# Performance work log

Measured on AMD Instinct MI355X. Metric: run time of the kernel, lower is better.

The kernel has to match this reference:

```python
import jax, jax.numpy as jnp
import numpy as np

N, E, SEQ, IN, HID, OUT = 2048, 65536, 5, 32, 64, 16
EPS = 1e-5


def setup_inputs() -> dict:
    ks = jax.random.split(jax.random.key(0), 16)
    def w(k, shape):
        return jax.random.normal(k, shape, jnp.float32) / np.float32(np.sqrt(shape[0]))
    z = lambda n: jnp.zeros((n,), jnp.float32)
    return dict(
        x=jax.random.normal(ks[0], (SEQ, N, IN), jnp.float32),
        edge_weight=jax.random.uniform(ks[1], (E,), jnp.float32),
        Wcz=w(ks[2], (IN, HID)), bcz=z(HID), Wlz=w(ks[3], (2 * HID, HID)), blz=z(HID),
        Wcr=w(ks[4], (IN, HID)), bcr=z(HID), Wlr=w(ks[5], (2 * HID, HID)), blr=z(HID),
        Wch=w(ks[6], (IN, HID)), bch=z(HID), Wlh=w(ks[7], (2 * HID, HID)), blh=z(HID),
        Wred=w(ks[8], (SEQ * HID, HID)), bred=z(HID),
        Wc1=w(ks[9], (HID, HID)), bc1=z(HID), Wc2=w(ks[10], (HID, HID)), bc2=z(HID),
        g1=jnp.ones((HID,), jnp.float32), be1=z(HID),
        g2=jnp.ones((HID,), jnp.float32), be2=z(HID),
        Wout=w(ks[11], (HID, OUT)), bout=z(OUT),
        Wi1=w(ks[12], (2 * HID, HID)), bi1=z(HID),
        Wi2=w(ks[13], (HID, 1)), bi2=z(1),
        edge_index=jax.random.randint(ks[14], (2, E), 0, N),
    )


def _layer_norm(h, g, b):
    mu = jnp.mean(h, -1, keepdims=True)
    var = jnp.mean((h - mu) ** 2, -1, keepdims=True)
    return (h - mu) * jax.lax.rsqrt(var + EPS) * g + b


def _forward(x, edge_weight, Wcz, bcz, Wlz, blz, Wcr, bcr, Wlr, blr,
             Wch, bch, Wlh, blh, Wred, bred, Wc1, bc1, Wc2, bc2,
             g1, be1, g2, be2, Wout, bout, Wi1, bi1, Wi2, bi2, edge_index):
    src, dst = edge_index[0], edge_index[1]
    # GCN symmetric normalization with self-loops (weight 1.0); shared by all convs.
    deg = jax.ops.segment_sum(edge_weight, dst, num_segments=N) + 1.0
    dinv = jax.lax.rsqrt(deg)
    norm = dinv[src] * edge_weight * dinv[dst]  # [E]
    dself = dinv * dinv                          # [N] self-loop coefficient

    def gcn(h, W, b):
        hw = h @ W
        agg = jax.ops.segment_sum(norm[:, None] * hw[src], dst, num_segments=N)
        return agg + dself[:, None] * hw + b

    # TGCN per timestep. The original passes no hidden state, so H resets to 0
    # each call: H_t = (1 - Z) * tanh(candidate); reset gate R is multiplied by
    # H=0 and has no effect (its params get zero gradient, matching torch).
    hs = []
    for t in range(SEQ):  # SEQ=5, fixed small loop
        Zg = jax.nn.sigmoid(gcn(x[t], Wcz, bcz) @ Wlz[:HID] + blz)
        Ht = jnp.tanh(gcn(x[t], Wch, bch) @ Wlh[:HID] + blh)
        hs.append((1.0 - Zg) * Ht)
    h = jnp.stack(hs, axis=1).reshape(N, SEQ * HID)
    h = h @ Wred + bred
    emb = h  # intermediate embeddings for the interaction predictor
    h = gcn(h, Wc1, bc1)
    h = jax.nn.relu(_layer_norm(h, g1, be1))  # dropout = identity in eval
    h = gcn(h, Wc2, bc2)
    h = jax.nn.relu(_layer_norm(h, g2, be2))
    node_pred = h @ Wout + bout
    # InteractionPredictor: cat([e_i, e_j]) @ Wi1 == e_i @ Wi1[:H] + e_j @ Wi1[H:]
    a = emb @ Wi1[:HID]
    bj = emb @ Wi1[HID:]
    hp = jax.nn.relu(a[:, None, :] + bj[None, :, :] + bi1)  # [N, N, HID]
    scores = (hp @ Wi2)[..., 0] + bi2[0]                     # [N, N]
    return node_pred, scores


def reference(x, edge_index, edge_weight, Wcz, bcz, Wlz, blz, Wcr, bcr, Wlr, blr,
              Wch, bch, Wlh, blh, Wred, bred, Wc1, bc1, Wc2, bc2,
              g1, be1, g2, be2, Wout, bout, Wi1, bi1, Wi2, bi2):
    return _forward(x, edge_weight, Wcz, bcz, Wlz, blz, Wcr, bcr, Wlr, blr,
                    Wch, bch, Wlh, blh, Wred, bred, Wc1, bc1, Wc2, bc2,
                    g1, be1, g2, be2, Wout, bout, Wi1, bi1, Wi2, bi2, edge_index)
```

## Files before the change

kernel.cpp:

```cpp
#include <hip/hip_runtime.h>
#include <math.h>

#define N_NODES 2048
#define N_EDGES 65536
#define SEQL 5
#define IN_F 32
#define HID 64
#define OUT_F 16
#define LN_EPS 1e-5f
#define CAP 128

__global__ __launch_bounds__(256) void k_build(
        const int* __restrict__ ei, const float* __restrict__ ew,
        const float* __restrict__ Wcz, const float* __restrict__ Wlz,
        const float* __restrict__ bcz, const float* __restrict__ blz,
        const float* __restrict__ Wch, const float* __restrict__ Wlh,
        const float* __restrict__ bch, const float* __restrict__ blh,
        float* __restrict__ deg, int* __restrict__ cnt, float2* __restrict__ cedge,
        float* __restrict__ Wzp, float* __restrict__ Whp, float* __restrict__ bUV){
    int b = blockIdx.x, t = threadIdx.x;
    if (b < 256){
        int e = b * 256 + t;
        int s = ei[e], d = ei[N_EDGES + e];
        float wv = ew[e];
        atomicAdd(&deg[d], wv);
        int pos = atomicAdd(&cnt[d], 1);
        if (pos < CAP){
            float2 v;
            v.x = __int_as_float(s);
            v.y = wv;
            cedge[(d << 7) + pos] = v;
        }
    } else {
        const float* Wc = (b == 256) ? Wcz : Wch;
        const float* Wl = (b == 256) ? Wlz : Wlh;
        const float* bc = (b == 256) ? bcz : bch;
        const float* bl = (b == 256) ? blz : blh;
        float* Wp = (b == 256) ? Wzp : Whp;
        for (int idx = t; idx < IN_F*HID; idx += 256){
            int i = idx >> 6, f = idx & 63;
            float s = 0.f;
            #pragma unroll 8
            for (int k = 0; k < HID; ++k) s += Wc[i*HID+k] * Wl[k*HID+f];
            Wp[idx] = s;
        }
        if (t < HID){
            float s = bl[t];
            for (int k = 0; k < HID; ++k) s += bc[k] * Wl[k*HID+t];
            bUV[(b-256)*HID + t] = s;
        }
    }
}

__global__ __launch_bounds__(320) void k_gate(const float* __restrict__ x,
        const float* __restrict__ deg, const int* __restrict__ cnt,
        const float2* __restrict__ cedge,
        const float* __restrict__ bUV, const float* __restrict__ Wzp, const float* __restrict__ Whp,
        const float* __restrict__ Wred, const float* __restrict__ bred,
        const float* __restrict__ Wi1, const float* __restrict__ bi1, const float* __restrict__ Wc1,
        float* __restrict__ ag, float* __restrict__ bjp, float* __restrict__ hw1y){
    int n = blockIdx.x;
    int tid = threadIdx.x;
    __shared__ float part[40*SEQL*IN_F];
    __shared__ float axs[SEQL][IN_F];
    __shared__ float hs[SEQL][HID];
    __shared__ float pw[SEQL][HID];
    __shared__ float hemb[HID];
    const int slot = tid >> 3, fl = tid & 7;
    const int f = tid & 63, t = tid >> 6;
    int m = min(cnt[n], CAP);
    float dvn = 1.f / sqrtf(deg[n] + 1.f);
    float dsn = dvn * dvn;
    const float4* X4 = (const float4*)x;
    float4 a0 = {0,0,0,0}, a1 = {0,0,0,0}, a2 = {0,0,0,0}, a3 = {0,0,0,0}, a4 = {0,0,0,0};
    for (int p = slot; p < m; p += 40){
        float2 ed = cedge[(n << 7) + p];
        int s = __float_as_int(ed.x);
        float c = ed.y * (1.f / sqrtf(deg[s] + 1.f));
        float4 x0 = X4[(0*N_NODES + s)*8 + fl];
        float4 x1 = X4[(1*N_NODES + s)*8 + fl];
        float4 x2 = X4[(2*N_NODES + s)*8 + fl];
        float4 x3 = X4[(3*N_NODES + s)*8 + fl];
        float4 x4v= X4[(4*N_NODES + s)*8 + fl];
        a0.x += c*x0.x; a0.y += c*x0.y; a0.z += c*x0.z; a0.w += c*x0.w;
        a1.x += c*x1.x; a1.y += c*x1.y; a1.z += c*x1.z; a1.w += c*x1.w;
        a2.x += c*x2.x; a2.y += c*x2.y; a2.z += c*x2.z; a2.w += c*x2.w;
        a3.x += c*x3.x; a3.y += c*x3.y; a3.z += c*x3.z; a3.w += c*x3.w;
        a4.x += c*x4v.x; a4.y += c*x4v.y; a4.z += c*x4v.z; a4.w += c*x4v.w;
    }
    *(float4*)&part[(slot*SEQL + 0)*IN_F + fl*4] = a0;
    *(float4*)&part[(slot*SEQL + 1)*IN_F + fl*4] = a1;
    *(float4*)&part[(slot*SEQL + 2)*IN_F + fl*4] = a2;
    *(float4*)&part[(slot*SEQL + 3)*IN_F + fl*4] = a3;
    *(float4*)&part[(slot*SEQL + 4)*IN_F + fl*4] = a4;
    __syncthreads();
    if (tid < SEQL*IN_F){
        int tt = tid >> 5, ff = tid & 31;
        float ps = 0.f;
        #pragma unroll 8
        for (int sl = 0; sl < 40; ++sl) ps += part[(sl*SEQL + tt)*IN_F + ff];
        axs[tt][ff] = dsn * x[(tt*N_NODES + n)*IN_F + ff] + dvn * ps;
    }
    __syncthreads();
    {
        float zz = bUV[f], hh = bUV[HID + f];
        #pragma unroll
        for (int i = 0; i < IN_F; ++i){
            float a = axs[t][i];
            zz += a * Wzp[i*HID + f];
            hh += a * Whp[i*HID + f];
        }
        float z = 1.f / (1.f + expf(-zz));
        hs[t][f] = (1.f - z) * tanhf(hh);
    }
    __syncthreads();
    {   float pp = 0.f;
        #pragma unroll
        for (int k = 0; k < HID; ++k) pp += hs[t][k] * Wred[(t*HID + k)*HID + f];
        pw[t][f] = pp;
    }
    __syncthreads();
    if (tid < HID){
        float hr = bred[tid];
        #pragma unroll
        for (int t2 = 0; t2 < SEQL; ++t2) hr += pw[t2][tid];
        hemb[tid] = hr;
    }
    __syncthreads();
    if (t < 3){
        const float* W = (t == 0) ? Wi1 : (t == 1) ? (Wi1 + HID*HID) : Wc1;
        float acc = (t == 1) ? bi1[f] : 0.f;
        #pragma unroll
        for (int k = 0; k < HID; ++k) acc += hemb[k] * W[k*HID + f];
        if (t == 2) acc *= dvn;
        float* O = (t == 0) ? ag : (t == 1) ? bjp : hw1y;
        O[n*HID + f] = acc;
    }
}

__global__ __launch_bounds__(512) void k_gcn1s(
        const float* __restrict__ hw1y, const float* __restrict__ deg,
        const int* __restrict__ cnt, const float2* __restrict__ cedge,
        const float* __restrict__ bc1, const float* __restrict__ g1, const float* __restrict__ be1,
        const float* __restrict__ Wc2, float* __restrict__ hw2y,
        const float* __restrict__ ag, const float* __restrict__ bjp,
        const float* __restrict__ Wi2, const float* __restrict__ bi2,
        float* __restrict__ outs){
    int blk = blockIdx.x;
    int tid = threadIdx.x;
    if (blk < 256){
        int w = tid >> 6, l = tid & 63;
        int n = (blk << 3) + w;
        int slot = l >> 4, fl = l & 15;
        int m = min(cnt[n], CAP);
        float dv = 1.f / sqrtf(deg[n] + 1.f);
        const float4* H4 = (const float4*)hw1y;
        float4 acc = {0.f,0.f,0.f,0.f};
        if (slot == 0) acc = H4[n*16 + fl];
        for (int p = slot; p < m; p += 4){
            float2 ed = cedge[(n << 7) + p];
            int s = __float_as_int(ed.x); float c = ed.y;
            float4 h = H4[s*16 + fl];
            acc.x += c*h.x; acc.y += c*h.y; acc.z += c*h.z; acc.w += c*h.w;
        }
        acc.x += __shfl_xor(acc.x, 16); acc.y += __shfl_xor(acc.y, 16);
        acc.z += __shfl_xor(acc.z, 16); acc.w += __shfl_xor(acc.w, 16);
        acc.x += __shfl_xor(acc.x, 32); acc.y += __shfl_xor(acc.y, 32);
        acc.z += __shfl_xor(acc.z, 32); acc.w += __shfl_xor(acc.w, 32);
        float4 b4 = ((const float4*)bc1)[fl];
        float4 g;
        g.x = b4.x + dv*acc.x; g.y = b4.y + dv*acc.y;
        g.z = b4.z + dv*acc.z; g.w = b4.w + dv*acc.w;
        float s4 = g.x + g.y + g.z + g.w;
        s4 += __shfl_xor(s4, 1); s4 += __shfl_xor(s4, 2);
        s4 += __shfl_xor(s4, 4); s4 += __shfl_xor(s4, 8);
        float mu = s4 * (1.f/64.f);
        float4 d;
        d.x = g.x - mu; d.y = g.y - mu; d.z = g.z - mu; d.w = g.w - mu;
        float v4 = d.x*d.x + d.y*d.y + d.z*d.z + d.w*d.w;
        v4 += __shfl_xor(v4, 1); v4 += __shfl_xor(v4, 2);
        v4 += __shfl_xor(v4, 4); v4 += __shfl_xor(v4, 8);
        float rs = 1.f / sqrtf(v4 * (1.f/64.f) + LN_EPS);
        float4 gm = ((const float4*)g1)[fl], be = ((const float4*)be1)[fl];
        float4 h4;
        h4.x = fmaxf(d.x*rs*gm.x + be.x, 0.f);
        h4.y = fmaxf(d.y*rs*gm.y + be.y, 0.f);
        h4.z = fmaxf(d.z*rs*gm.z + be.z, 0.f);
        h4.w = fmaxf(d.w*rs*gm.w + be.w, 0.f);
        float o = 0.f;
        #pragma unroll 4
        for (int gk = 0; gk < 16; ++gk){
            float hb0 = __shfl(h4.x, gk);
            float hb1 = __shfl(h4.y, gk);
            float hb2 = __shfl(h4.z, gk);
            float hb3 = __shfl(h4.w, gk);
            o += hb0 * Wc2[(4*gk+0)*HID + l];
            o += hb1 * Wc2[(4*gk+1)*HID + l];
            o += hb2 * Wc2[(4*gk+2)*HID + l];
            o += hb3 * Wc2[(4*gk+3)*HID + l];
        }
        hw2y[n*HID + l] = dv * o;
    } else {
        __shared__ float bs[64*65];
        __shared__ float wv[64];
        int tl = blk - 256;
        int j0 = (tl & 31) * 64;
        int i0 = (tl >> 5) * 32;
        for (int idx = tid; idx < 4096; idx += 512){
            int jj = idx >> 6, f = idx & 63;
            bs[jj*65 + f] = bjp[(j0 + jj)*HID + f];
        }
        if (tid < 64) wv[tid] = Wi2[tid];
        __syncthreads();
        int tj = tid & 63;
        int w = __builtin_amdgcn_readfirstlane(tid >> 6);
        const float* ar = ag + (i0 + w*4)*HID;
        float bi2v = bi2[0];
        float acc0 = 0.f, acc1 = 0.f, acc2 = 0.f, acc3 = 0.f;
        #pragma unroll
        for (int f = 0; f < 64; ++f){
            float bv = bs[tj*65 + f];
            float wf = wv[f];
            acc0 += fmaxf(ar[       f] + bv, 0.f) * wf;
            acc1 += fmaxf(ar[ 64 +  f] + bv, 0.f) * wf;
            acc2 += fmaxf(ar[128 +  f] + bv, 0.f) * wf;
            acc3 += fmaxf(ar[192 +  f] + bv, 0.f) * wf;
        }
        long ro = (long)(i0 + w*4) * N_NODES + j0 + tj;
        outs[ro                ] = acc0 + bi2v;
        outs[ro +     N_NODES  ] = acc1 + bi2v;
        outs[ro + 2L* N_NODES  ] = acc2 + bi2v;
        outs[ro + 3L* N_NODES  ] = acc3 + bi2v;
    }
}

__global__ __launch_bounds__(512) void k_gcn2s(
        const float* __restrict__ hw2y, const float* __restrict__ deg,
        const int* __restrict__ cnt, const float2* __restrict__ cedge,
        const float* __restrict__ bc2, const float* __restrict__ g2, const float* __restrict__ be2,
        const float* __restrict__ Wout, const float* __restrict__ bout,
        const float* __restrict__ ag, const float* __restrict__ bjp,
        const float* __restrict__ Wi2, const float* __restrict__ bi2,
        float* __restrict__ outp, float* __restrict__ outs){
    int blk = blockIdx.x;
    int tid = threadIdx.x;
    if (blk < 256){
        int w = tid >> 6, l = tid & 63;
        int n = (blk << 3) + w;
        int slot = l >> 4, fl = l & 15;
        int m = min(cnt[n], CAP);
        float dv = 1.f / sqrtf(deg[n] + 1.f);
        const float4* H4 = (const float4*)hw2y;
        float4 acc = {0.f,0.f,0.f,0.f};
        if (slot == 0) acc = H4[n*16 + fl];
        for (int p = slot; p < m; p += 4){
            float2 ed = cedge[(n << 7) + p];
            int s = __float_as_int(ed.x); float c = ed.y;
            float4 h = H4[s*16 + fl];
            acc.x += c*h.x; acc.y += c*h.y; acc.z += c*h.z; acc.w += c*h.w;
        }
        acc.x += __shfl_xor(acc.x, 16); acc.y += __shfl_xor(acc.y, 16);
        acc.z += __shfl_xor(acc.z, 16); acc.w += __shfl_xor(acc.w, 16);
        acc.x += __shfl_xor(acc.x, 32); acc.y += __shfl_xor(acc.y, 32);
        acc.z += __shfl_xor(acc.z, 32); acc.w += __shfl_xor(acc.w, 32);
        float4 b4 = ((const float4*)bc2)[fl];
        float4 g;
        g.x = b4.x + dv*acc.x; g.y = b4.y + dv*acc.y;
        g.z = b4.z + dv*acc.z; g.w = b4.w + dv*acc.w;
        float s4 = g.x + g.y + g.z + g.w;
        s4 += __shfl_xor(s4, 1); s4 += __shfl_xor(s4, 2);
        s4 += __shfl_xor(s4, 4); s4 += __shfl_xor(s4, 8);
        float mu = s4 * (1.f/64.f);
        float4 d;
        d.x = g.x - mu; d.y = g.y - mu; d.z = g.z - mu; d.w = g.w - mu;
        float v4 = d.x*d.x + d.y*d.y + d.z*d.z + d.w*d.w;
        v4 += __shfl_xor(v4, 1); v4 += __shfl_xor(v4, 2);
        v4 += __shfl_xor(v4, 4); v4 += __shfl_xor(v4, 8);
        float rs = 1.f / sqrtf(v4 * (1.f/64.f) + LN_EPS);
        float4 gm = ((const float4*)g2)[fl], be = ((const float4*)be2)[fl];
        float4 h4;
        h4.x = fmaxf(d.x*rs*gm.x + be.x, 0.f);
        h4.y = fmaxf(d.y*rs*gm.y + be.y, 0.f);
        h4.z = fmaxf(d.z*rs*gm.z + be.z, 0.f);
        h4.w = fmaxf(d.w*rs*gm.w + be.w, 0.f);
        int f2 = l & 15;
        float o = bout[f2];
        #pragma unroll 4
        for (int gk = 0; gk < 16; ++gk){
            float hb0 = __shfl(h4.x, gk);
            float hb1 = __shfl(h4.y, gk);
            float hb2 = __shfl(h4.z, gk);
            float hb3 = __shfl(h4.w, gk);
            o += hb0 * Wout[(4*gk+0)*OUT_F + f2];
            o += hb1 * Wout[(4*gk+1)*OUT_F + f2];
            o += hb2 * Wout[(4*gk+2)*OUT_F + f2];
            o += hb3 * Wout[(4*gk+3)*OUT_F + f2];
        }
        if (slot == 0) outp[n*OUT_F + f2] = o;
    } else {
        __shared__ float bs[64*65];
        __shared__ float wv[64];
        int tl = blk - 256 + 1024;
        int j0 = (tl & 31) * 64;
        int i0 = (tl >> 5) * 32;
        for (int idx = tid; idx < 4096; idx += 512){
            int jj = idx >> 6, f = idx & 63;
            bs[jj*65 + f] = bjp[(j0 + jj)*HID + f];
        }
        if (tid < 64) wv[tid] = Wi2[tid];
        __syncthreads();
        int tj = tid & 63;
        int w = __builtin_amdgcn_readfirstlane(tid >> 6);
        const float* ar = ag + (i0 + w*4)*HID;
        float bi2v = bi2[0];
        float acc0 = 0.f, acc1 = 0.f, acc2 = 0.f, acc3 = 0.f;
        #pragma unroll
        for (int f = 0; f < 64; ++f){
            float bv = bs[tj*65 + f];
            float wf = wv[f];
            acc0 += fmaxf(ar[       f] + bv, 0.f) * wf;
            acc1 += fmaxf(ar[ 64 +  f] + bv, 0.f) * wf;
            acc2 += fmaxf(ar[128 +  f] + bv, 0.f) * wf;
            acc3 += fmaxf(ar[192 +  f] + bv, 0.f) * wf;
        }
        long ro = (long)(i0 + w*4) * N_NODES + j0 + tj;
        outs[ro                ] = acc0 + bi2v;
        outs[ro +     N_NODES  ] = acc1 + bi2v;
        outs[ro + 2L* N_NODES  ] = acc2 + bi2v;
        outs[ro + 3L* N_NODES  ] = acc3 + bi2v;
    }
}

extern "C" void kernel_launch(void* const* d_in, const int* in_sizes, int n_in,
                              void* d_out, int out_size, void* d_ws, size_t ws_size,
                              hipStream_t stream){
    const float* x   = (const float*)d_in[0];
    const float* ew  = (const float*)d_in[1];
    const float* Wcz = (const float*)d_in[2];  const float* bcz = (const float*)d_in[3];
    const float* Wlz = (const float*)d_in[4];  const float* blz = (const float*)d_in[5];
    const float* Wch = (const float*)d_in[10]; const float* bch = (const float*)d_in[11];
    const float* Wlh = (const float*)d_in[12]; const float* blh = (const float*)d_in[13];
    const float* Wred= (const float*)d_in[14]; const float* bred= (const float*)d_in[15];
    const float* Wc1 = (const float*)d_in[16]; const float* bc1 = (const float*)d_in[17];
    const float* Wc2 = (const float*)d_in[18]; const float* bc2 = (const float*)d_in[19];
    const float* g1  = (const float*)d_in[20]; const float* be1 = (const float*)d_in[21];
    const float* g2  = (const float*)d_in[22]; const float* be2 = (const float*)d_in[23];
    const float* Wout= (const float*)d_in[24]; const float* bout= (const float*)d_in[25];
    const float* Wi1 = (const float*)d_in[26]; const float* bi1 = (const float*)d_in[27];
    const float* Wi2 = (const float*)d_in[28]; const float* bi2 = (const float*)d_in[29];
    const int*  ei  = (const int*)d_in[30];

    float* w = (float*)d_ws;
    float* deg   = w;
    int*   cnt   = (int*)(w + 2048);
    float2* cedge= (float2*)(w + 4096);
    float* Wzp   = w + 528384;
    float* Whp   = w + 530432;
    float* bUV   = w + 532480;
    float* ag    = w + 532608;
    float* bjp   = w + 663680;
    float* hw1y  = w + 794752;
    float* hw2y  = w + 925824;

    hipMemsetAsync(deg, 0, 16384, stream);
    k_build<<<258, 256, 0, stream>>>(ei, ew, Wcz, Wlz, bcz, blz, Wch, Wlh, bch, blh,
                                     deg, cnt, cedge, Wzp, Whp, bUV);
    k_gate<<<N_NODES, 320, 0, stream>>>(x, deg, cnt, cedge, bUV, Wzp, Whp,
                                        Wred, bred, Wi1, bi1, Wc1, ag, bjp, hw1y);
    k_gcn1s<<<256 + 1024, 512, 0, stream>>>(hw1y, deg, cnt, cedge, bc1, g1, be1,
                                            Wc2, hw2y, ag, bjp, Wi2, bi2,
                                            (float*)d_out + N_NODES*OUT_F);
    k_gcn2s<<<256 + 1024, 512, 0, stream>>>(hw2y, deg, cnt, cedge, bc2, g2, be2,
                                            Wout, bout, ag, bjp, Wi2, bi2,
                                            (float*)d_out, (float*)d_out + N_NODES*OUT_F);
}
```

Measured before the change: 198.4 us.

## Fuse four kernels into one persistent kernel with software grid barriers

Result: slower. 388.3 us (+95.7%).

```diff
diff --git a/kernel.cpp b/kernel.cpp
--- a/kernel.cpp
+++ b/kernel.cpp
@@ -9,18 +9,213 @@
 #define OUT_F 16
 #define LN_EPS 1e-5f
 #define CAP 128
-
-__global__ __launch_bounds__(256) void k_build(
-        const int* __restrict__ ei, const float* __restrict__ ew,
-        const float* __restrict__ Wcz, const float* __restrict__ Wlz,
-        const float* __restrict__ bcz, const float* __restrict__ blz,
-        const float* __restrict__ Wch, const float* __restrict__ Wlh,
-        const float* __restrict__ bch, const float* __restrict__ blh,
-        float* __restrict__ deg, int* __restrict__ cnt, float2* __restrict__ cedge,
-        float* __restrict__ Wzp, float* __restrict__ Whp, float* __restrict__ bUV){
-    int b = blockIdx.x, t = threadIdx.x;
-    if (b < 256){
-        int e = b * 256 + t;
+#define NBLK 512
+
+__device__ __forceinline__ void gbar(unsigned* bar, unsigned target){
+    __syncthreads();
+    if (threadIdx.x == 0){
+        __threadfence();
+        atomicAdd(bar, 1u);
+        while (atomicAdd(bar, 0u) < target) __builtin_amdgcn_s_sleep(2);
+        __threadfence();
+    }
+    __syncthreads();
+}
+
+union SMem {
+    struct {
+        float part[2][16][SEQL][IN_F];
+        float axs[2][SEQL][IN_F];
+        float hs[2][SEQL][HID];
+        float pw[2][SEQL][HID];
+        float hemb[2][HID];
+    } g;
+    struct { float bs[64*65]; float wv[64]; } s;
+};
+
+__device__ __forceinline__ void score_tile(int tl, int tid, SMem& sm,
+        const float* __restrict__ ag, const float* __restrict__ bjp,
+        const float* __restrict__ Wi2, const float* __restrict__ bi2,
+        float* __restrict__ outs){
+    int j0 = (tl & 31) * 64;
+    int i0 = (tl >> 5) * 32;
+    __syncthreads();
+    for (int idx = tid; idx < 4096; idx += 256){
+        int jj = idx >> 6, f = idx & 63;
+        sm.s.bs[jj*65 + f] = bjp[(j0 + jj)*HID + f];
+    }
+    if (tid < 64) sm.s.wv[tid] = Wi2[tid];
+    __syncthreads();
+    int tj = tid & 63;
+    int w = __builtin_amdgcn_readfirstlane(tid >> 6);
+    const float* ar = ag + (i0 + w*8)*HID;
+    float bi2v = bi2[0];
+    float a0=0.f,a1=0.f,a2=0.f,a3=0.f,a4=0.f,a5=0.f,a6=0.f,a7=0.f;
+    #pragma unroll 16
+    for (int f = 0; f < 64; ++f){
+        float bv = sm.s.bs[tj*65 + f];
+        float wf = sm.s.wv[f];
+        a0 += fmaxf(ar[0*HID + f] + bv, 0.f) * wf;
+        a1 += fmaxf(ar[1*HID + f] + bv, 0.f) * wf;
+        a2 += fmaxf(ar[2*HID + f] + bv, 0.f) * wf;
+        a3 += fmaxf(ar[3*HID + f] + bv, 0.f) * wf;
+        a4 += fmaxf(ar[4*HID + f] + bv, 0.f) * wf;
+        a5 += fmaxf(ar[5*HID + f] + bv, 0.f) * wf;
+        a6 += fmaxf(ar[6*HID + f] + bv, 0.f) * wf;
+        a7 += fmaxf(ar[7*HID + f] + bv, 0.f) * wf;
+    }
+    long ro = (long)(i0 + w*8) * N_NODES + j0 + tj;
+    outs[ro              ] = a0 + bi2v;
+    outs[ro + 1L*N_NODES ] = a1 + bi2v;
+    outs[ro + 2L*N_NODES ] = a2 + bi2v;
+    outs[ro + 3L*N_NODES ] = a3 + bi2v;
+    outs[ro + 4L*N_NODES ] = a4 + bi2v;
+    outs[ro + 5L*N_NODES ] = a5 + bi2v;
+    outs[ro + 6L*N_NODES ] = a6 + bi2v;
+    outs[ro + 7L*N_NODES ] = a7 + bi2v;
+}
+
+__device__ __forceinline__ void gcn1_node(int n, int l,
+        const float* __restrict__ deg, const int* __restrict__ cnt,
+        const float2* __restrict__ cedge, const float* __restrict__ hw1y,
+        const float* __restrict__ bc1, const float* __restrict__ g1,
+        const float* __restrict__ be1, const float* __restrict__ Wc2,
+        float* __restrict__ hw2y){
+    int slot = l >> 4, fl = l & 15;
+    int m = min(cnt[n], CAP);
+    float dv = 1.f / sqrtf(deg[n] + 1.f);
+    const float4* H4 = (const float4*)hw1y;
+    float4 acc = {0.f,0.f,0.f,0.f};
+    if (slot == 0) acc = H4[n*16 + fl];
+    for (int p = slot; p < m; p += 4){
+        float2 ed = cedge[(n << 7) + p];
+        int s = __float_as_int(ed.x); float c = ed.y;
+        float4 h = H4[s*16 + fl];
+        acc.x += c*h.x; acc.y += c*h.y; acc.z += c*h.z; acc.w += c*h.w;
+    }
+    acc.x += __shfl_xor(acc.x, 16); acc.y += __shfl_xor(acc.y, 16);
+    acc.z += __shfl_xor(acc.z, 16); acc.w += __shfl_xor(acc.w, 16);
+    acc.x += __shfl_xor(acc.x, 32); acc.y += __shfl_xor(acc.y, 32);
+    acc.z += __shfl_xor(acc.z, 32); acc.w += __shfl_xor(acc.w, 32);
+    float4 b4 = ((const float4*)bc1)[fl];
+    float4 g;
+    g.x = b4.x + dv*acc.x; g.y = b4.y + dv*acc.y;
+    g.z = b4.z + dv*acc.z; g.w = b4.w + dv*acc.w;
+    float s4 = g.x + g.y + g.z + g.w;
+    s4 += __shfl_xor(s4, 1); s4 += __shfl_xor(s4, 2);
+    s4 += __shfl_xor(s4, 4); s4 += __shfl_xor(s4, 8);
+    float mu = s4 * (1.f/64.f);
+    float4 d;
+    d.x = g.x - mu; d.y = g.y - mu; d.z = g.z - mu; d.w = g.w - mu;
+    float v4 = d.x*d.x + d.y*d.y + d.z*d.z + d.w*d.w;
+    v4 += __shfl_xor(v4, 1); v4 += __shfl_xor(v4, 2);
+    v4 += __shfl_xor(v4, 4); v4 += __shfl_xor(v4, 8);
+    float rs = 1.f / sqrtf(v4 * (1.f/64.f) + LN_EPS);
+    float4 gm = ((const float4*)g1)[fl], be = ((const float4*)be1)[fl];
+    float4 h4;
+    h4.x = fmaxf(d.x*rs*gm.x + be.x, 0.f);
+    h4.y = fmaxf(d.y*rs*gm.y + be.y, 0.f);
+    h4.z = fmaxf(d.z*rs*gm.z + be.z, 0.f);
+    h4.w = fmaxf(d.w*rs*gm.w + be.w, 0.f);
+    float o = 0.f;
+    #pragma unroll 4
+    for (int gk = 0; gk < 16; ++gk){
+        float hb0 = __shfl(h4.x, gk);
+        float hb1 = __shfl(h4.y, gk);
+        float hb2 = __shfl(h4.z, gk);
+        float hb3 = __shfl(h4.w, gk);
+        o += hb0 * Wc2[(4*gk+0)*HID + l];
+        o += hb1 * Wc2[(4*gk+1)*HID + l];
+        o += hb2 * Wc2[(4*gk+2)*HID + l];
+        o += hb3 * Wc2[(4*gk+3)*HID + l];
+    }
+    hw2y[n*HID + l] = dv * o;
+}
+
+__device__ __forceinline__ void gcn2_node(int n, int l,
+        const float* __restrict__ deg, const int* __restrict__ cnt,
+        const float2* __restrict__ cedge, const float* __restrict__ hw2y,
+        const float* __restrict__ bc2, const float* __restrict__ g2,
+        const float* __restrict__ be2, const float* __restrict__ Wout,
+        const float* __restrict__ bout, float* __restrict__ outp){
+    int slot = l >> 4, fl = l & 15;
+    int m = min(cnt[n], CAP);
+    float dv = 1.f / sqrtf(deg[n] + 1.f);
+    const float4* H4 = (const float4*)hw2y;
+    float4 acc = {0.f,0.f,0.f,0.f};
+    if (slot == 0) acc = H4[n*16 + fl];
+    for (int p = slot; p < m; p += 4){
+        float2 ed = cedge[(n << 7) + p];
+        int s = __float_as_int(ed.x); float c = ed.y;
+        float4 h = H4[s*16 + fl];
+        acc.x += c*h.x; acc.y += c*h.y; acc.z += c*h.z; acc.w += c*h.w;
+    }
+    acc.x += __shfl_xor(acc.x, 16); acc.y += __shfl_xor(acc.y, 16);
+    acc.z += __shfl_xor(acc.z, 16); acc.w += __shfl_xor(acc.w, 16);
+    acc.x += __shfl_xor(acc.x, 32); acc.y += __shfl_xor(acc.y, 32);
+    acc.z += __shfl_xor(acc.z, 32); acc.w += __shfl_xor(acc.w, 32);
+    float4 b4 = ((const float4*)bc2)[fl];
+    float4 g;
+    g.x = b4.x + dv*acc.x; g.y = b4.y + dv*acc.y;
+    g.z = b4.z + dv*acc.z; g.w = b4.w + dv*acc.w;
+    float s4 = g.x + g.y + g.z + g.w;
+    s4 += __shfl_xor(s4, 1); s4 += __shfl_xor(s4, 2);
+    s4 += __shfl_xor(s4, 4); s4 += __shfl_xor(s4, 8);
+    float mu = s4 * (1.f/64.f);
+    float4 d;
+    d.x = g.x - mu; d.y = g.y - mu; d.z = g.z - mu; d.w = g.w - mu;
+    float v4 = d.x*d.x + d.y*d.y + d.z*d.z + d.w*d.w;
+    v4 += __shfl_xor(v4, 1); v4 += __shfl_xor(v4, 2);
+    v4 += __shfl_xor(v4, 4); v4 += __shfl_xor(v4, 8);
+    float rs = 1.f / sqrtf(v4 * (1.f/64.f) + LN_EPS);
+    float4 gm = ((const float4*)g2)[fl], be = ((const float4*)be2)[fl];
+    float4 h4;
+    h4.x = fmaxf(d.x*rs*gm.x + be.x, 0.f);
+    h4.y = fmaxf(d.y*rs*gm.y + be.y, 0.f);
+    h4.z = fmaxf(d.z*rs*gm.z + be.z, 0.f);
+    h4.w = fmaxf(d.w*rs*gm.w + be.w, 0.f);
+    int f2 = l & 15;
+    float o = bout[f2];
+    #pragma unroll 4
+    for (int gk = 0; gk < 16; ++gk){
+        float hb0 = __shfl(h4.x, gk);
+        float hb1 = __shfl(h4.y, gk);
+        float hb2 = __shfl(h4.z, gk);
+        float hb3 = __shfl(h4.w, gk);
+        o += hb0 * Wout[(4*gk+0)*OUT_F + f2];
+        o += hb1 * Wout[(4*gk+1)*OUT_F + f2];
+        o += hb2 * Wout[(4*gk+2)*OUT_F + f2];
+        o += hb3 * Wout[(4*gk+3)*OUT_F + f2];
+    }
+    if (slot == 0) outp[n*OUT_F + f2] = o;
+}
+
+__global__ __launch_bounds__(256, 2) void k_mega(
+        const float* __restrict__ x, const float* __restrict__ ew, const int* __restrict__ ei,
+        const float* __restrict__ Wcz, const float* __restrict__ bcz,
+        const float* __restrict__ Wlz, const float* __restrict__ blz,
+        const float* __restrict__ Wch, const float* __restrict__ bch,
+        const float* __restrict__ Wlh, const float* __restrict__ blh,
+        const float* __restrict__ Wred, const float* __restrict__ bred,
+        const float* __restrict__ Wc1, const float* __restrict__ bc1,
+        const float* __restrict__ Wc2, const float* __restrict__ bc2,
+        const float* __restrict__ g1, const float* __restrict__ be1,
+        const float* __restrict__ g2, const float* __restrict__ be2,
+        const float* __restrict__ Wout, const float* __restrict__ bout,
+        const float* __restrict__ Wi1, const float* __restrict__ bi1,
+        const float* __restrict__ Wi2, const float* __restrict__ bi2,
+        float* __restrict__ deg, int* __restrict__ cnt, unsigned* __restrict__ bar,
+        float2* __restrict__ cedge,
+        float* __restrict__ Wzp, float* __restrict__ Whp, float* __restrict__ bUV,
+        float* __restrict__ ag, float* __restrict__ bjp,
+        float* __restrict__ hw1y, float* __restrict__ hw2y,
+        float* __restrict__ outp, float* __restrict__ outs){
+    __shared__ SMem sm;
+    const int blk = blockIdx.x, tid = threadIdx.x;
+    const int w = tid >> 6, l = tid & 63;
+
+    if (blk < 256){
+        int e = blk * 256 + tid;
         int s = ei[e], d = ei[N_EDGES + e];
         float wv = ew[e];
         atomicAdd(&deg[d], wv);
@@ -31,304 +226,145 @@
             v.y = wv;
             cedge[(d << 7) + pos] = v;
         }
-    } else {
-        const float* Wc = (b == 256) ? Wcz : Wch;
-        const float* Wl = (b == 256) ? Wlz : Wlh;
-        const float* bc = (b == 256) ? bcz : bch;
-        const float* bl = (b == 256) ? blz : blh;
-        float* Wp = (b == 256) ? Wzp : Whp;
-        for (int idx = t; idx < IN_F*HID; idx += 256){
+    } else if (blk < 258){
+        const float* Wc = (blk == 256) ? Wcz : Wch;
+        const float* Wl = (blk == 256) ? Wlz : Wlh;
+        float* Wp = (blk == 256) ? Wzp : Whp;
+        for (int idx = tid; idx < IN_F*HID; idx += 256){
             int i = idx >> 6, f = idx & 63;
             float s = 0.f;
             #pragma unroll 8
             for (int k = 0; k < HID; ++k) s += Wc[i*HID+k] * Wl[k*HID+f];
             Wp[idx] = s;
         }
-        if (t < HID){
-            float s = bl[t];
-            for (int k = 0; k < HID; ++k) s += bc[k] * Wl[k*HID+t];
-            bUV[(b-256)*HID + t] = s;
-        }
-    }
-}
-
-__global__ __launch_bounds__(320) void k_gate(const float* __restrict__ x,
-        const float* __restrict__ deg, const int* __restrict__ cnt,
-        const float2* __restrict__ cedge,
-        const float* __restrict__ bUV, const float* __restrict__ Wzp, const float* __restrict__ Whp,
-        const float* __restrict__ Wred, const float* __restrict__ bred,
-        const float* __restrict__ Wi1, const float* __restrict__ bi1, const float* __restrict__ Wc1,
-        float* __restrict__ ag, float* __restrict__ bjp, float* __restrict__ hw1y){
-    int n = blockIdx.x;
-    int tid = threadIdx.x;
-    __shared__ float part[40*SEQL*IN_F];
-    __shared__ float axs[SEQL][IN_F];
-    __shared__ float hs[SEQL][HID];
-    __shared__ float pw[SEQL][HID];
-    __shared__ float hemb[HID];
-    const int slot = tid >> 3, fl = tid & 7;
-    const int f = tid & 63, t = tid >> 6;
-    int m = min(cnt[n], CAP);
-    float dvn = 1.f / sqrtf(deg[n] + 1.f);
-    float dsn = dvn * dvn;
-    const float4* X4 = (const float4*)x;
-    float4 a0 = {0,0,0,0}, a1 = {0,0,0,0}, a2 = {0,0,0,0}, a3 = {0,0,0,0}, a4 = {0,0,0,0};
-    for (int p = slot; p < m; p += 40){
-        float2 ed = cedge[(n << 7) + p];
-        int s = __float_as_int(ed.x);
-        float c = ed.y * (1.f / sqrtf(deg[s] + 1.f));
-        float4 x0 = X4[(0*N_NODES + s)*8 + fl];
-        float4 x1 = X4[(1*N_NODES + s)*8 + fl];
-        float4 x2 = X4[(2*N_NODES + s)*8 + fl];
-        float4 x3 = X4[(3*N_NODES + s)*8 + fl];
-        float4 x4v= X4[(4*N_NODES + s)*8 + fl];
-        a0.x += c*x0.x; a0.y += c*x0.y; a0.z += c*x0.z; a0.w += c*x0.w;
-        a1.x += c*x1.x; a1.y += c*x1.y; a1.z += c*x1.z; a1.w += c*x1.w;
-        a2.x += c*x2.x; a2.y += c*x2.y; a2.z += c*x2.z; a2.w += c*x2.w;
-        a3.x += c*x3.x; a3.y += c*x3.y; a3.z += c*x3.z; a3.w += c*x3.w;
-        a4.x += c*x4v.x; a4.y += c*x4v.y; a4.z += c*x4v.z; a4.w += c*x4v.w;
-    }
-    *(float4*)&part[(slot*SEQL + 0)*IN_F + fl*4] = a0;
-    *(float4*)&part[(slot*SEQL + 1)*IN_F + fl*4] = a1;
-    *(float4*)&part[(slot*SEQL + 2)*IN_F + fl*4] = a2;
-    *(float4*)&part[(slot*SEQL + 3)*IN_F + fl*4] = a3;
-    *(float4*)&part[(slot*SEQL + 4)*IN_F + fl*4] = a4;
-    __syncthreads();
-    if (tid < SEQL*IN_F){
-        int tt = tid >> 5, ff = tid & 31;
-        float ps = 0.f;
-        #pragma unroll 8
-        for (int sl = 0; sl < 40; ++sl) ps += part[(sl*SEQL + tt)*IN_F + ff];
-        axs[tt][ff] = dsn * x[(tt*N_NODES + n)*IN_F + ff] + dvn * ps;
-    }
-    __syncthreads();
-    {
-        float zz = bUV[f], hh = bUV[HID + f];
-        #pragma unroll
-        for (int i = 0; i < IN_F; ++i){
-            float a = axs[t][i];
-            zz += a * Wzp[i*HID + f];
-            hh += a * Whp[i*HID + f];
-        }
-        float z = 1.f / (1.f + expf(-zz));
-        hs[t][f] = (1.f - z) * tanhf(hh);
-    }
-    __syncthreads();
-    {   float pp = 0.f;
-        #pragma unroll
-        for (int k = 0; k < HID; ++k) pp += hs[t][k] * Wred[(t*HID + k)*HID + f];
-        pw[t][f] = pp;
-    }
-    __syncthreads();
-    if (tid < HID){
-        float hr = bred[tid];
-        #pragma unroll
-        for (int t2 = 0; t2 < SEQL; ++t2) hr += pw[t2][tid];
-        hemb[tid] = hr;
-    }
-    __syncthreads();
-    if (t < 3){
-        const float* W = (t == 0) ? Wi1 : (t == 1) ? (Wi1 + HID*HID) : Wc1;
-        float acc = (t == 1) ? bi1[f] : 0.f;
-        #pragma unroll
-        for (int k = 0; k < HID; ++k) acc += hemb[k] * W[k*HID + f];
-        if (t == 2) acc *= dvn;
-        float* O = (t == 0) ? ag : (t == 1) ? bjp : hw1y;
-        O[n*HID + f] = acc;
-    }
-}
-
-__global__ __launch_bounds__(512) void k_gcn1s(
-        const float* __restrict__ hw1y, const float* __restrict__ deg,
-        const int* __restrict__ cnt, const float2* __restrict__ cedge,
-        const float* __restrict__ bc1, const float* __restrict__ g1, const float* __restrict__ be1,
-        const float* __restrict__ Wc2, float* __restrict__ hw2y,
-        const float* __restrict__ ag, const float* __restrict__ bjp,
-        const float* __restrict__ Wi2, const float* __restrict__ bi2,
-        float* __restrict__ outs){
-    int blk = blockIdx.x;
-    int tid = threadIdx.x;
+    } else if (blk == 258){
+        if (tid < 128){
+            int which = tid >> 6, f = tid & 63;
+            const float* Wl = which ? Wlh : Wlz;
+            const float* bc = which ? bch : bcz;
+            const float* bl = which ? blh : blz;
+            float s = bl[f];
+            for (int k = 0; k < HID; ++k) s += bc[k] * Wl[k*HID+f];
+            bUV[which*HID + f] = s;
+        }
+    }
+    gbar(bar, NBLK);
+
+    for (int pass = 0; pass < 2; ++pass){
+        int nb = (blk << 2) + pass*2;
+        {
+            int half = tid >> 7;
+            int r = tid & 127;
+            int slot = r >> 3, fl = r & 7;
+            int n = nb + half;
+            int m = min(cnt[n], CAP);
+            const float4* X4 = (const float4*)x;
+            float4 a0={0,0,0,0},a1={0,0,0,0},a2={0,0,0,0},a3={0,0,0,0},a4={0,0,0,0};
+            for (int p = slot; p < m; p += 16){
+                float2 edv = cedge[(n << 7) + p];
+                int s = __float_as_int(edv.x);
+                float c = edv.y * (1.f / sqrtf(deg[s] + 1.f));
+                float4 x0 = X4[(0*N_NODES + s)*8 + fl];
+                float4 x1 = X4[(1*N_NODES + s)*8 + fl];
+                float4 x2 = X4[(2*N_NODES + s)*8 + fl];
+                float4 x3 = X4[(3*N_NODES + s)*8 + fl];
+                float4 x4v= X4[(4*N_NODES + s)*8 + fl];
+                a0.x += c*x0.x; a0.y += c*x0.y; a0.z += c*x0.z; a0.w += c*x0.w;
+                a1.x += c*x1.x; a1.y += c*x1.y; a1.z += c*x1.z; a1.w += c*x1.w;
+                a2.x += c*x2.x; a2.y += c*x2.y; a2.z += c*x2.z; a2.w += c*x2.w;
+                a3.x += c*x3.x; a3.y += c*x3.y; a3.z += c*x3.z; a3.w += c*x3.w;
+                a4.x += c*x4v.x; a4.y += c*x4v.y; a4.z += c*x4v.z; a4.w += c*x4v.w;
+            }
+            *(float4*)&sm.g.part[half][slot][0][fl*4] = a0;
+            *(float4*)&sm.g.part[half][slot][1][fl*4] = a1;
+            *(float4*)&sm.g.part[half][slot][2][fl*4] = a2;
+            *(float4*)&sm.g.part[half][slot][3][fl*4] = a3;
+            *(float4*)&sm.g.part[half][slot][4][fl*4] = a4;
+        }
+        __syncthreads();
+        for (int idx = tid; idx < 2*SEQL*IN_F; idx += 256){
+            int nn = idx >= 160 ? 1 : 0;
+            int rem = idx - nn*160;
+            int tt = rem >> 5, ff = rem & 31;
+            int n = nb + nn;
+            float dv = 1.f / sqrtf(deg[n] + 1.f);
+            float ps = 0.f;
+            #pragma unroll
+            for (int sl = 0; sl < 16; ++sl) ps += sm.g.part[nn][sl][tt][ff];
+            sm.g.axs[nn][tt][ff] = dv*dv * x[(tt*N_NODES + n)*IN_F + ff] + dv * ps;
+        }
+        __syncthreads();
+        for (int task = w; task < 10; task += 4){
+            int nn = task >= 5 ? 1 : 0;
+            int t = task - nn*5;
+            float zz = bUV[l], hh = bUV[HID + l];
+            #pragma unroll 8
+            for (int i = 0; i < IN_F; ++i){
+                float a = sm.g.axs[nn][t][i];
+                zz += a * Wzp[i*HID + l];
+                hh += a * Whp[i*HID + l];
+            }
+            float z = 1.f / (1.f + expf(-zz));
+            sm.g.hs[nn][t][l] = (1.f - z) * tanhf(hh);
+        }
+        __syncthreads();
+        for (int task = w; task < 10; task += 4){
+            int nn = task >= 5 ? 1 : 0;
+            int t = task - nn*5;
+            float pp = 0.f;
+            #pragma unroll 8
+            for (int k = 0; k < HID; ++k) pp += sm.g.hs[nn][t][k] * Wred[(t*HID + k)*HID + l];
+            sm.g.pw[nn][t][l] = pp;
+        }
+        __syncthreads();
+        if (tid < 2*HID){
+            int nn = tid >> 6, ff = tid & 63;
+            float hr = bred[ff];
+            #pragma unroll
+            for (int t2 = 0; t2 < SEQL; ++t2) hr += sm.g.pw[nn][t2][ff];
+            sm.g.hemb[nn][ff] = hr;
+        }
+        __syncthreads();
+        for (int task = w; task < 6; task += 4){
+            int nn = task >= 3 ? 1 : 0;
+            int o = task - nn*3;
+            int n = nb + nn;
+            const float* W = (o == 0) ? Wi1 : (o == 1) ? (Wi1 + HID*HID) : Wc1;
+            float acc = (o == 1) ? bi1[l] : 0.f;
+            #pragma unroll 8
+            for (int k = 0; k < HID; ++k) acc += sm.g.hemb[nn][k] * W[k*HID + l];
+            if (o == 2) acc *= 1.f / sqrtf(deg[n] + 1.f);
+            float* O = (o == 0) ? ag : (o == 1) ? bjp : hw1y;
+            O[n*HID + l] = acc;
+        }
+        __syncthreads();
+    }
+    gbar(bar, 2*NBLK);
+
     if (blk < 256){
-        int w = tid >> 6, l = tid & 63;
-        int n = (blk << 3) + w;
-        int slot = l >> 4, fl = l & 15;
-        int m = min(cnt[n], CAP);
-        float dv = 1.f / sqrtf(deg[n] + 1.f);
-        const float4* H4 = (const float4*)hw1y;
-        float4 acc = {0.f,0.f,0.f,0.f};
-        if (slot == 0) acc = H4[n*16 + fl];
-        for (int p = slot; p < m; p += 4){
-            float2 ed = cedge[(n << 7) + p];
-            int s = __float_as_int(ed.x); float c = ed.y;
-            float4 h = H4[s*16 + fl];
-            acc.x += c*h.x; acc.y += c*h.y; acc.z += c*h.z; acc.w += c*h.w;
-        }
-        acc.x += __shfl_xor(acc.x, 16); acc.y += __shfl_xor(acc.y, 16);
-        acc.z += __shfl_xor(acc.z, 16); acc.w += __shfl_xor(acc.w, 16);
-        acc.x += __shfl_xor(acc.x, 32); acc.y += __shfl_xor(acc.y, 32);
-        acc.z += __shfl_xor(acc.z, 32); acc.w += __shfl_xor(acc.w, 32);
-        float4 b4 = ((const float4*)bc1)[fl];
-        float4 g;
-        g.x = b4.x + dv*acc.x; g.y = b4.y + dv*acc.y;
-        g.z = b4.z + dv*acc.z; g.w = b4.w + dv*acc.w;
-        float s4 = g.x + g.y + g.z + g.w;
-        s4 += __shfl_xor(s4, 1); s4 += __shfl_xor(s4, 2);
-        s4 += __shfl_xor(s4, 4); s4 += __shfl_xor(s4, 8);
-        float mu = s4 * (1.f/64.f);
-        float4 d;
-        d.x = g.x - mu; d.y = g.y - mu; d.z = g.z - mu; d.w = g.w - mu;
-        float v4 = d.x*d.x + d.y*d.y + d.z*d.z + d.w*d.w;
-        v4 += __shfl_xor(v4, 1); v4 += __shfl_xor(v4, 2);
-        v4 += __shfl_xor(v4, 4); v4 += __shfl_xor(v4, 8);
-        float rs = 1.f / sqrtf(v4 * (1.f/64.f) + LN_EPS);
-        float4 gm = ((const float4*)g1)[fl], be = ((const float4*)be1)[fl];
-        float4 h4;
-        h4.x = fmaxf(d.x*rs*gm.x + be.x, 0.f);
-        h4.y = fmaxf(d.y*rs*gm.y + be.y, 0.f);
-        h4.z = fmaxf(d.z*rs*gm.z + be.z, 0.f);
-        h4.w = fmaxf(d.w*rs*gm.w + be.w, 0.f);
-        float o = 0.f;
-        #pragma unroll 4
-        for (int gk = 0; gk < 16; ++gk){
-            float hb0 = __shfl(h4.x, gk);
-            float hb1 = __shfl(h4.y, gk);
-            float hb2 = __shfl(h4.z, gk);
-            float hb3 = __shfl(h4.w, gk);
-            o += hb0 * Wc2[(4*gk+0)*HID + l];
-            o += hb1 * Wc2[(4*gk+1)*HID + l];
-            o += hb2 * Wc2[(4*gk+2)*HID + l];
-            o += hb3 * Wc2[(4*gk+3)*HID + l];
-        }
-        hw2y[n*HID + l] = dv * o;
+        for (int rep = 0; rep < 2; ++rep){
+            int n = (blk << 3) + rep*4 + w;
+            gcn1_node(n, l, deg, cnt, cedge, hw1y, bc1, g1, be1, Wc2, hw2y);
+        }
     } else {
-        __shared__ float bs[64*65];
-        __shared__ float wv[64];
-        int tl = blk - 256;
-        int j0 = (tl & 31) * 64;
-        int i0 = (tl >> 5) * 32;
-        for (int idx = tid; idx < 4096; idx += 512){
-            int jj = idx >> 6, f = idx & 63;
-            bs[jj*65 + f] = bjp[(j0 + jj)*HID + f];
-        }
-        if (tid < 64) wv[tid] = Wi2[tid];
-        __syncthreads();
-        int tj = tid & 63;
-        int w = __builtin_amdgcn_readfirstlane(tid >> 6);
-        const float* ar = ag + (i0 + w*4)*HID;
-        float bi2v = bi2[0];
-        float acc0 = 0.f, acc1 = 0.f, acc2 = 0.f, acc3 = 0.f;
-        #pragma unroll
-        for (int f = 0; f < 64; ++f){
-            float bv = bs[tj*65 + f];
-            float wf = wv[f];
-            acc0 += fmaxf(ar[       f] + bv, 0.f) * wf;
-            acc1 += fmaxf(ar[ 64 +  f] + bv, 0.f) * wf;
-            acc2 += fmaxf(ar[128 +  f] + bv, 0.f) * wf;
-            acc3 += fmaxf(ar[192 +  f] + bv, 0.f) * wf;
-        }
-        long ro = (long)(i0 + w*4) * N_NODES + j0 + tj;
-        outs[ro                ] = acc0 + bi2v;
-        outs[ro +     N_NODES  ] = acc1 + bi2v;
-        outs[ro + 2L* N_NODES  ] = acc2 + bi2v;
-        outs[ro + 3L* N_NODES  ] = acc3 + bi2v;
-    }
-}
-
-__global__ __launch_bounds__(512) void k_gcn2s(
-        const float* __restrict__ hw2y, const float* __restrict__ deg,
-        const int* __restrict__ cnt, const float2* __restrict__ cedge,
-        const float* __restrict__ bc2, const float* __restrict__ g2, const float* __restrict__ be2,
-        const float* __restrict__ Wout, const float* __restrict__ bout,
-        const float* __restrict__ ag, const float* __restrict__ bjp,
-        const float* __restrict__ Wi2, const float* __restrict__ bi2,
-        float* __restrict__ outp, float* __restrict__ outs){
-    int blk = blockIdx.x;
-    int tid = threadIdx.x;
+        score_tile((blk - 256)*2,     tid, sm, ag, bjp, Wi2, bi2, outs);
+        score_tile((blk - 256)*2 + 1, tid, sm, ag, bjp, Wi2, bi2, outs);
+    }
+    gbar(bar, 3*NBLK);
+
     if (blk < 256){
-        int w = tid >> 6, l = tid & 63;
-        int n = (blk << 3) + w;
-        int slot = l >> 4, fl = l & 15;
-        int m = min(cnt[n], CAP);
-        float dv = 1.f / sqrtf(deg[n] + 1.f);
-        const float4* H4 = (const float4*)hw2y;
-        float4 acc = {0.f,0.f,0.f,0.f};
-        if (slot == 0) acc = H4[n*16 + fl];
-        for (int p = slot; p < m; p += 4){
-            float2 ed = cedge[(n << 7) + p];
-            int s = __float_as_int(ed.x); float c = ed.y;
-            float4 h = H4[s*16 + fl];
-            acc.x += c*h.x; acc.y += c*h.y; acc.z += c*h.z; acc.w += c*h.w;
-        }
-        acc.x += __shfl_xor(acc.x, 16); acc.y += __shfl_xor(acc.y, 16);
-        acc.z += __shfl_xor(acc.z, 16); acc.w += __shfl_xor(acc.w, 16);
-        acc.x += __shfl_xor(acc.x, 32); acc.y += __shfl_xor(acc.y, 32);
-        acc.z += __shfl_xor(acc.z, 32); acc.w += __shfl_xor(acc.w, 32);
-        float4 b4 = ((const float4*)bc2)[fl];
-        float4 g;
-        g.x = b4.x + dv*acc.x; g.y = b4.y + dv*acc.y;
-        g.z = b4.z + dv*acc.z; g.w = b4.w + dv*acc.w;
-        float s4 = g.x + g.y + g.z + g.w;
-        s4 += __shfl_xor(s4, 1); s4 += __shfl_xor(s4, 2);
-        s4 += __shfl_xor(s4, 4); s4 += __shfl_xor(s4, 8);
-        float mu = s4 * (1.f/64.f);
-        float4 d;
-        d.x = g.x - mu; d.y = g.y - mu; d.z = g.z - mu; d.w = g.w - mu;
-        float v4 = d.x*d.x + d.y*d.y + d.z*d.z + d.w*d.w;
-        v4 += __shfl_xor(v4, 1); v4 += __shfl_xor(v4, 2);
-        v4 += __shfl_xor(v4, 4); v4 += __shfl_xor(v4, 8);
-        float rs = 1.f / sqrtf(v4 * (1.f/64.f) + LN_EPS);
-        float4 gm = ((const float4*)g2)[fl], be = ((const float4*)be2)[fl];
-        float4 h4;
-        h4.x = fmaxf(d.x*rs*gm.x + be.x, 0.f);
-        h4.y = fmaxf(d.y*rs*gm.y + be.y, 0.f);
-        h4.z = fmaxf(d.z*rs*gm.z + be.z, 0.f);
-        h4.w = fmaxf(d.w*rs*gm.w + be.w, 0.f);
-        int f2 = l & 15;
-        float o = bout[f2];
-        #pragma unroll 4
-        for (int gk = 0; gk < 16; ++gk){
-            float hb0 = __shfl(h4.x, gk);
-            float hb1 = __shfl(h4.y, gk);
-            float hb2 = __shfl(h4.z, gk);
-            float hb3 = __shfl(h4.w, gk);
-            o += hb0 * Wout[(4*gk+0)*OUT_F + f2];
-            o += hb1 * Wout[(4*gk+1)*OUT_F + f2];
-            o += hb2 * Wout[(4*gk+2)*OUT_F + f2];
-            o += hb3 * Wout[(4*gk+3)*OUT_F + f2];
-        }
-        if (slot == 0) outp[n*OUT_F + f2] = o;
+        for (int rep = 0; rep < 2; ++rep){
+            int n = (blk << 3) + rep*4 + w;
+            gcn2_node(n, l, deg, cnt, cedge, hw2y, bc2, g2, be2, Wout, bout, outp);
+        }
     } else {
-        __shared__ float bs[64*65];
-        __shared__ float wv[64];
-        int tl = blk - 256 + 1024;
-        int j0 = (tl & 31) * 64;
-        int i0 = (tl >> 5) * 32;
-        for (int idx = tid; idx < 4096; idx += 512){
-            int jj = idx >> 6, f = idx & 63;
-            bs[jj*65 + f] = bjp[(j0 + jj)*HID + f];
-        }
-        if (tid < 64) wv[tid] = Wi2[tid];
-        __syncthreads();
-        int tj = tid & 63;
-        int w = __builtin_amdgcn_readfirstlane(tid >> 6);
-        const float* ar = ag + (i0 + w*4)*HID;
-        float bi2v = bi2[0];
-        float acc0 = 0.f, acc1 = 0.f, acc2 = 0.f, acc3 = 0.f;
-        #pragma unroll
-        for (int f = 0; f < 64; ++f){
-            float bv = bs[tj*65 + f];
-            float wf = wv[f];
-            acc0 += fmaxf(ar[       f] + bv, 0.f) * wf;
-            acc1 += fmaxf(ar[ 64 +  f] + bv, 0.f) * wf;
-            acc2 += fmaxf(ar[128 +  f] + bv, 0.f) * wf;
-            acc3 += fmaxf(ar[192 +  f] + bv, 0.f) * wf;
-        }
-        long ro = (long)(i0 + w*4) * N_NODES + j0 + tj;
-        outs[ro                ] = acc0 + bi2v;
-        outs[ro +     N_NODES  ] = acc1 + bi2v;
-        outs[ro + 2L* N_NODES  ] = acc2 + bi2v;
-        outs[ro + 3L* N_NODES  ] = acc3 + bi2v;
-    }
+        score_tile(512 + (blk - 256), tid, sm, ag, bjp, Wi2, bi2, outs);
+    }
+
+    score_tile(768 + blk,        tid, sm, ag, bjp, Wi2, bi2, outs);
+    score_tile(768 + NBLK + blk, tid, sm, ag, bjp, Wi2, bi2, outs);
+    if (blk < 256)
+        score_tile(768 + 2*NBLK + blk, tid, sm, ag, bjp, Wi2, bi2, outs);
 }
 
 extern "C" void kernel_launch(void* const* d_in, const int* in_sizes, int n_in,
@@ -353,24 +389,21 @@
     float* w = (float*)d_ws;
     float* deg   = w;
     int*   cnt   = (int*)(w + 2048);
-    float2* cedge= (float2*)(w + 4096);
-    float* Wzp   = w + 528384;
-    float* Whp   = w + 530432;
-    float* bUV   = w + 532480;
-    float* ag    = w + 532608;
-    float* bjp   = w + 663680;
-    float* hw1y  = w + 794752;
-    float* hw2y  = w + 925824;
-
-    hipMemsetAsync(deg, 0, 16384, stream);
-    k_build<<<258, 256, 0, stream>>>(ei, ew, Wcz, Wlz, bcz, blz, Wch, Wlh, bch, blh,
-                                     deg, cnt, cedge, Wzp, Whp, bUV);
-    k_gate<<<N_NODES, 320, 0, stream>>>(x, deg, cnt, cedge, bUV, Wzp, Whp,
-                                        Wred, bred, Wi1, bi1, Wc1, ag, bjp, hw1y);
-    k_gcn1s<<<256 + 1024, 512, 0, stream>>>(hw1y, deg, cnt, cedge, bc1, g1, be1,
-                                            Wc2, hw2y, ag, bjp, Wi2, bi2,
-                                            (float*)d_out + N_NODES*OUT_F);
-    k_gcn2s<<<256 + 1024, 512, 0, stream>>>(hw2y, deg, cnt, cedge, bc2, g2, be2,
-                                            Wout, bout, ag, bjp, Wi2, bi2,
-                                            (float*)d_out, (float*)d_out + N_NODES*OUT_F);
-}
+    unsigned* bar= (unsigned*)(w + 4096);
+    float2* cedge= (float2*)(w + 4112);
+    float* Wzp   = w + 528400;
+    float* Whp   = w + 530448;
+    float* bUV   = w + 532496;
+    float* ag    = w + 532624;
+    float* bjp   = w + 663696;
+    float* hw1y  = w + 794768;
+    float* hw2y  = w + 925840;
+    float* outp  = (float*)d_out;
+    float* outs  = (float*)d_out + N_NODES*OUT_F;
+
+    hipMemsetAsync(deg, 0, 16448, stream);
+    k_mega<<<NBLK, 256, 0, stream>>>(x, ew, ei,
+        Wcz, bcz, Wlz, blz, Wch, bch, Wlh, blh, Wred, bred,
+        Wc1, bc1, Wc2, bc2, g1, be1, g2, be2, Wout, bout, Wi1, bi1, Wi2, bi2,
+        deg, cnt, bar, cedge, Wzp, Whp, bUV, ag, bjp, hw1y, hw2y, outp, outs);
+}
```

## Split gate kernel into gather and batched dense kernel with LDS-staged weights

Applied to the files above, without the earlier changes.

Result: no change. 196.2 us, median of 2 (-1.1%).

```diff
diff --git a/kernel.cpp b/kernel.cpp
--- a/kernel.cpp
+++ b/kernel.cpp
@@ -52,25 +52,14 @@
     }
 }
 
-__global__ __launch_bounds__(320) void k_gate(const float* __restrict__ x,
+__global__ __launch_bounds__(320) void k_gather(const float* __restrict__ x,
         const float* __restrict__ deg, const int* __restrict__ cnt,
-        const float2* __restrict__ cedge,
-        const float* __restrict__ bUV, const float* __restrict__ Wzp, const float* __restrict__ Whp,
-        const float* __restrict__ Wred, const float* __restrict__ bred,
-        const float* __restrict__ Wi1, const float* __restrict__ bi1, const float* __restrict__ Wc1,
-        float* __restrict__ ag, float* __restrict__ bjp, float* __restrict__ hw1y){
+        const float2* __restrict__ cedge, float* __restrict__ axs_out){
     int n = blockIdx.x;
     int tid = threadIdx.x;
     __shared__ float part[40*SEQL*IN_F];
-    __shared__ float axs[SEQL][IN_F];
-    __shared__ float hs[SEQL][HID];
-    __shared__ float pw[SEQL][HID];
-    __shared__ float hemb[HID];
     const int slot = tid >> 3, fl = tid & 7;
-    const int f = tid & 63, t = tid >> 6;
     int m = min(cnt[n], CAP);
-    float dvn = 1.f / sqrtf(deg[n] + 1.f);
-    float dsn = dvn * dvn;
     const float4* X4 = (const float4*)x;
     float4 a0 = {0,0,0,0}, a1 = {0,0,0,0}, a2 = {0,0,0,0}, a3 = {0,0,0,0}, a4 = {0,0,0,0};
     for (int p = slot; p < m; p += 40){
@@ -96,46 +85,75 @@
     __syncthreads();
     if (tid < SEQL*IN_F){
         int tt = tid >> 5, ff = tid & 31;
+        float dvn = 1.f / sqrtf(deg[n] + 1.f);
         float ps = 0.f;
         #pragma unroll 8
         for (int sl = 0; sl < 40; ++sl) ps += part[(sl*SEQL + tt)*IN_F + ff];
-        axs[tt][ff] = dsn * x[(tt*N_NODES + n)*IN_F + ff] + dvn * ps;
+        axs_out[n*(SEQL*IN_F) + tid] = dvn*dvn * x[(tt*N_NODES + n)*IN_F + ff] + dvn * ps;
+    }
+}
+
+__global__ __launch_bounds__(512) void k_dense(const float* __restrict__ axs_in,
+        const float* __restrict__ deg,
+        const float* __restrict__ Wzp, const float* __restrict__ Whp,
+        const float* __restrict__ bUV,
+        const float* __restrict__ Wred, const float* __restrict__ bred,
+        const float* __restrict__ Wi1, const float* __restrict__ bi1,
+        const float* __restrict__ Wc1,
+        float* __restrict__ ag, float* __restrict__ bjp, float* __restrict__ hw1y){
+    __shared__ float wl[4096];
+    __shared__ float axsf[8*SEQL*IN_F];
+    __shared__ float hsf[8*SEQL*HID];
+    __shared__ float hembf[8*HID];
+    int tid = threadIdx.x;
+    int w = tid >> 6, l = tid & 63;
+    int n = (blockIdx.x << 3) + w;
+    axsf[w*160 + l]      = axs_in[n*160 + l];
+    axsf[w*160 + 64 + l] = axs_in[n*160 + 64 + l];
+    if (l < 32) axsf[w*160 + 128 + l] = axs_in[n*160 + 128 + l];
+    for (int idx = tid; idx < 2048; idx += 512){
+        wl[idx]        = Wzp[idx];
+        wl[2048 + idx] = Whp[idx];
     }
     __syncthreads();
-    {
-        float zz = bUV[f], hh = bUV[HID + f];
-        #pragma unroll
+    float bz = bUV[l], bh = bUV[HID + l];
+    #pragma unroll
+    for (int t = 0; t < SEQL; ++t){
+        float zz = bz, hh = bh;
+        #pragma unroll 8
         for (int i = 0; i < IN_F; ++i){
-            float a = axs[t][i];
-            zz += a * Wzp[i*HID + f];
-            hh += a * Whp[i*HID + f];
+            float a = axsf[w*160 + t*32 + i];
+            zz += a * wl[i*HID + l];
+            hh += a * wl[2048 + i*HID + l];
         }
         float z = 1.f / (1.f + expf(-zz));
-        hs[t][f] = (1.f - z) * tanhf(hh);
-    }
-    __syncthreads();
-    {   float pp = 0.f;
-        #pragma unroll
-        for (int k = 0; k < HID; ++k) pp += hs[t][k] * Wred[(t*HID + k)*HID + f];
-        pw[t][f] = pp;
-    }
-    __syncthreads();
-    if (tid < HID){
-        float hr = bred[tid];
-        #pragma unroll
-        for (int t2 = 0; t2 < SEQL; ++t2) hr += pw[t2][tid];
-        hemb[tid] = hr;
-    }
-    __syncthreads();
-    if (t < 3){
-        const float* W = (t == 0) ? Wi1 : (t == 1) ? (Wi1 + HID*HID) : Wc1;
-        float acc = (t == 1) ? bi1[f] : 0.f;
-        #pragma unroll
-        for (int k = 0; k < HID; ++k) acc += hemb[k] * W[k*HID + f];
-        if (t == 2) acc *= dvn;
-        float* O = (t == 0) ? ag : (t == 1) ? bjp : hw1y;
-        O[n*HID + f] = acc;
-    }
+        hsf[w*320 + t*64 + l] = (1.f - z) * tanhf(hh);
+    }
+    float hr = bred[l];
+    for (int t = 0; t < SEQL; ++t){
+        __syncthreads();
+        for (int idx = tid; idx < 4096; idx += 512) wl[idx] = Wred[t*4096 + idx];
+        __syncthreads();
+        #pragma unroll 8
+        for (int k = 0; k < HID; ++k)
+            hr += hsf[w*320 + t*64 + k] * wl[k*HID + l];
+    }
+    hembf[w*HID + l] = hr;
+    float rA, rB, rC;
+    #pragma unroll
+    for (int o = 0; o < 3; ++o){
+        __syncthreads();
+        const float* W = (o == 0) ? Wi1 : (o == 1) ? (Wi1 + HID*HID) : Wc1;
+        for (int idx = tid; idx < 4096; idx += 512) wl[idx] = W[idx];
+        __syncthreads();
+        float acc = (o == 1) ? bi1[l] : 0.f;
+        #pragma unroll 8
+        for (int k = 0; k < HID; ++k) acc += hembf[w*HID + k] * wl[k*HID + l];
+        if (o == 0) rA = acc; else if (o == 1) rB = acc; else rC = acc;
+    }
+    ag  [n*HID + l] = rA;
+    bjp [n*HID + l] = rB;
+    hw1y[n*HID + l] = rC * (1.f / sqrtf(deg[n] + 1.f));
 }
 
 __global__ __launch_bounds__(512) void k_gcn1s(
@@ -361,12 +379,14 @@
     float* bjp   = w + 663680;
     float* hw1y  = w + 794752;
     float* hw2y  = w + 925824;
+    float* axs   = w + 1056896;
 
     hipMemsetAsync(deg, 0, 16384, stream);
     k_build<<<258, 256, 0, stream>>>(ei, ew, Wcz, Wlz, bcz, blz, Wch, Wlh, bch, blh,
                                      deg, cnt, cedge, Wzp, Whp, bUV);
-    k_gate<<<N_NODES, 320, 0, stream>>>(x, deg, cnt, cedge, bUV, Wzp, Whp,
-                                        Wred, bred, Wi1, bi1, Wc1, ag, bjp, hw1y);
+    k_gather<<<N_NODES, 320, 0, stream>>>(x, deg, cnt, cedge, axs);
+    k_dense<<<256, 512, 0, stream>>>(axs, deg, Wzp, Whp, bUV, Wred, bred,
+                                     Wi1, bi1, Wc1, ag, bjp, hw1y);
     k_gcn1s<<<256 + 1024, 512, 0, stream>>>(hw1y, deg, cnt, cedge, bc1, g1, be1,
                                             Wc2, hw2y, ag, bjp, Wi2, bi2,
                                             (float*)d_out + N_NODES*OUT_F);
```
